# Optimization experiments

Hardware: AMD Instinct MI355X
Metric: run time of the kernel (lower is better)

Reference implementation:

```python
import jax, jax.numpy as jnp
import numpy as np

B, DIM, IMG, HEADS, DH = 8, 512, 32, 8, 64
INNER = HEADS * DH  # == DIM, required by final reshape(b, n, c)
N = IMG * IMG
BN_EPS = 1e-5


def setup_inputs() -> dict:
    key = jax.random.key(0)
    ks = jax.random.split(key, 11)
    s = lambda k, sh: jax.random.normal(k, sh, jnp.float32) * 0.05
    return {
        "x": jax.random.normal(ks[0], (B, N, DIM), jnp.float32),
        # stacked q/k/v params, index 0=q, 1=k, 2=v
        "dw_w": s(ks[1], (3, DIM, 1, 3, 3)),   # depthwise conv kernels (OIHW, groups=DIM)
        "dw_b": s(ks[2], (3, DIM)),
        "bn_g": jnp.ones((3, DIM), jnp.float32) + s(ks[3], (3, DIM)),
        "bn_b": s(ks[4], (3, DIM)),
        "bn_m": s(ks[5], (3, DIM)),
        "bn_v": jnp.abs(jax.random.normal(ks[6], (3, DIM), jnp.float32)) + 1.0,
        "pw_w": s(ks[7], (3, INNER, DIM)),     # pointwise 1x1 conv weights
        "pw_b": s(ks[8], (3, INNER)),
        "out_w": s(ks[9], (DIM, INNER)),       # nn.Linear weight [out, in]
        "out_b": s(ks[10], (DIM,)),
    }


def _proj(x_img, dw_w, dw_b, bn_g, bn_b, bn_m, bn_v, pw_w, pw_b):
    # depthwise 3x3 conv, stride 1, pad 1
    y = jax.lax.conv_general_dilated(
        x_img, dw_w, (1, 1), [(1, 1), (1, 1)],
        dimension_numbers=("NCHW", "OIHW", "NCHW"), feature_group_count=DIM)
    y = y + dw_b[None, :, None, None]
    # eval-mode BatchNorm2d
    scale = bn_g / jnp.sqrt(bn_v + BN_EPS)
    y = (y - bn_m[None, :, None, None]) * scale[None, :, None, None] + bn_b[None, :, None, None]
    # pointwise 1x1 conv
    y = jnp.einsum("bchw,oc->bohw", y, pw_w) + pw_b[None, :, None, None]
    return y


def reference(x, dw_w, dw_b, bn_g, bn_b, bn_m, bn_v, pw_w, pw_b, out_w, out_b):
    b = x.shape[0]
    # b (l w) c -> b c l w
    xi = x.transpose(0, 2, 1).reshape(b, DIM, IMG, IMG)
    # q, k, v: b (h d) l w -> b h (l w) d
    qkv = [
        _proj(xi, dw_w[i], dw_b[i], bn_g[i], bn_b[i], bn_m[i], bn_v[i], pw_w[i], pw_b[i])
        .reshape(b, HEADS, DH, N).transpose(0, 1, 3, 2)
        for i in range(3)
    ]
    q, k, v = qkv
    att = jax.nn.softmax(jnp.einsum("bhnd,bhmd->bhnm", q, k) * (DH ** -0.5), axis=-1)
    out = jnp.einsum("bhnm,bhmd->bhnd", att, v)  # [b,h,n,d]
    out = out.transpose(0, 2, 1, 3).reshape(b, N, INNER)
    return out @ out_w.T + out_b  # to_out Linear (dropout=0)
```

## Files before the change

kernel.cpp:

```cpp
#include <hip/hip_runtime.h>
#include <hip/hip_bf16.h>

#define BB    8
#define DIMC  512
#define IMGS  32
#define NPIX  1024
#define NHEAD 8
#define DHEAD 64

typedef __attribute__((ext_vector_type(8))) short short8;
typedef __attribute__((ext_vector_type(4))) float float4v;

__device__ __forceinline__ float b2f(unsigned short u) {
  union { unsigned int i; float f; } c;
  c.i = ((unsigned int)u) << 16;
  return c.f;
}
__device__ __forceinline__ unsigned short f2b(float f) {
  union { float f; unsigned int u; } c;
  c.f = f;
  unsigned int r = c.u + 0x7fffu + ((c.u >> 16) & 1u);
  return (unsigned short)(r >> 16);
}

__device__ __forceinline__ void storeC(float* p, float v) { *p = v; }
__device__ __forceinline__ void storeC(unsigned short* p, float v) { *p = f2b(v); }

__device__ __forceinline__ void async16(const void* g, void* l) {
  __builtin_amdgcn_global_load_lds(
      (const __attribute__((address_space(1))) void*)g,
      (__attribute__((address_space(3))) void*)l, 16, 0, 0);
}

#define WAITCNT_VM0   0x0F70
#define WAITCNT_LGKM0 0xC07F

__global__ __launch_bounds__(256) void wcvt_kernel(
    const float* __restrict__ pw_w, const float* __restrict__ out_w,
    const float* __restrict__ pw_b, const float* __restrict__ dw_w,
    const float* __restrict__ dw_b, const float* __restrict__ bn_g,
    const float* __restrict__ bn_b, const float* __restrict__ bn_m,
    const float* __restrict__ bn_v, unsigned short* __restrict__ wbf,
    float* __restrict__ bb, float* __restrict__ wT,
    float* __restrict__ shiftv) {
  const int i4 = (blockIdx.x * 256 + threadIdx.x) * 4;
  float4 v = (i4 < 3 * DIMC * DIMC)
                 ? *reinterpret_cast<const float4*>(pw_w + i4)
                 : *reinterpret_cast<const float4*>(out_w + (i4 - 3 * DIMC * DIMC));
  const float sc = (i4 < DIMC * DIMC) ? 0.125f : 1.0f;
  ushort4 o;
  o.x = f2b(v.x * sc); o.y = f2b(v.y * sc); o.z = f2b(v.z * sc); o.w = f2b(v.w * sc);
  *reinterpret_cast<ushort4*>(wbf + i4) = o;
  const int idx = blockIdx.x * 256 + threadIdx.x;
  if (idx < 6 * 256) {
    if (idx < 3 * DIMC / 2) {
      #pragma unroll
      for (int hh = 0; hh < 2; ++hh) {
        const int id2 = idx * 2 + hh;
        const int i = id2 >> 9, c = id2 & 511;
        const float scale = bn_g[id2] * rsqrtf(bn_v[id2] + 1e-5f);
        shiftv[id2] = (dw_b[id2] - bn_m[id2]) * scale + bn_b[id2];
        #pragma unroll
        for (int t = 0; t < 9; ++t)
          wT[(i * 9 + t) * DIMC + c] = dw_w[(size_t)id2 * 9 + t] * scale;
      }
    }
    #pragma unroll
    for (int k = 0; k < 1; ++k) {
      if (idx < 3 * DIMC)
        bb[idx] = pw_b[idx] * (idx < DIMC ? 0.125f : 1.0f);
    }
  }
}

__global__ __launch_bounds__(256) void dwbn_kernel(
    const float* __restrict__ x, const float* __restrict__ wT,
    const float* __restrict__ shiftv, unsigned short* __restrict__ z) {
  const int wp = blockIdx.x, lg = blockIdx.y, b = blockIdx.z;
  const int t = threadIdx.x;
  const int c = (t & 127) * 4;
  const int w = wp * 2 + (t >> 7);
  const int l0 = lg * 4;
  const float* xb = x + (size_t)b * NPIX * DIMC + c;

  const float4 zero4 = make_float4(0.f, 0.f, 0.f, 0.f);
  float4 win[6][3];
  #pragma unroll
  for (int rr = 0; rr < 6; ++rr) {
    const int l = l0 - 1 + rr;
    #pragma unroll
    for (int dw = 0; dw < 3; ++dw) {
      const int ww = w - 1 + dw;
      const bool ok = ((unsigned)l < IMGS) && ((unsigned)ww < IMGS);
      win[rr][dw] = ok ? *reinterpret_cast<const float4*>(
                             xb + (size_t)(l * IMGS + ww) * DIMC)
                       : zero4;
    }
  }

  #pragma unroll
  for (int i = 0; i < 3; ++i) {
    float4 wv[9];
    #pragma unroll
    for (int tp = 0; tp < 9; ++tp)
      wv[tp] = *reinterpret_cast<const float4*>(wT + (i * 9 + tp) * DIMC + c);
    const float4 sh = *reinterpret_cast<const float4*>(shiftv + i * DIMC + c);
    #pragma unroll
    for (int r = 0; r < 4; ++r) {
      float a0 = sh.x, a1 = sh.y, a2 = sh.z, a3 = sh.w;
      #pragma unroll
      for (int kh = 0; kh < 3; ++kh)
        #pragma unroll
        for (int kw = 0; kw < 3; ++kw) {
          const float4 wq = wv[kh * 3 + kw];
          const float4 xq = win[r + kh][kw];
          a0 = fmaf(wq.x, xq.x, a0);
          a1 = fmaf(wq.y, xq.y, a1);
          a2 = fmaf(wq.z, xq.z, a2);
          a3 = fmaf(wq.w, xq.w, a3);
        }
      ushort4 st;
      st.x = f2b(a0); st.y = f2b(a1); st.z = f2b(a2); st.w = f2b(a3);
      *reinterpret_cast<ushort4*>(
          z + (((size_t)(i * BB + b)) * NPIX + (l0 + r) * IMGS + w) * DIMC + c) = st;
    }
  }
}

template <typename CT>
__global__ __launch_bounds__(256) void gemm_mfma(
    const unsigned short* __restrict__ Abase,
    const unsigned short* __restrict__ Wbase,
    const float* __restrict__ biasBase, CT* __restrict__ Cbase) {
  __shared__ short As[8 * 64 * 8];
  __shared__ short Bs[8 * 64 * 8];
  const int bz = blockIdx.z;
  const int wi = bz >> 3;
  const short* A = (const short*)Abase + (size_t)bz * NPIX * DIMC;
  const short* W = (const short*)Wbase + (size_t)wi * DIMC * DIMC;
  const float* bias = biasBase + wi * DIMC;
  CT* C = Cbase + (size_t)bz * NPIX * DIMC;

  const int t = threadIdx.x;
  const int wv = t >> 6, lane = t & 63;
  const int lo = lane & 15, hi = lane >> 4;
  const int wm = wv >> 1, wn = wv & 1;
  const int m0 = blockIdx.y * 128, n0 = blockIdx.x * 128;

  float4v acc[4][4];
  #pragma unroll
  for (int i = 0; i < 4; ++i)
    #pragma unroll
    for (int j = 0; j < 4; ++j) acc[i][j] = {0.f, 0.f, 0.f, 0.f};

  for (int k0 = 0; k0 < DIMC; k0 += 32) {
    #pragma unroll
    for (int p = 0; p < 2; ++p) {
      const int sub = wv + p * 4;
      async16(A + (size_t)(m0 + sub * 16 + lo) * DIMC + k0 + hi * 8,
              As + (sub * 64 + lane) * 8);
      async16(W + (size_t)(n0 + sub * 16 + lo) * DIMC + k0 + hi * 8,
              Bs + (sub * 64 + lane) * 8);
    }
    __syncthreads();
    short8 af[4], bf[4];
    #pragma unroll
    for (int mt = 0; mt < 4; ++mt)
      af[mt] = *reinterpret_cast<const short8*>(As + ((wm * 4 + mt) * 64 + lane) * 8);
    #pragma unroll
    for (int nt = 0; nt < 4; ++nt)
      bf[nt] = *reinterpret_cast<const short8*>(Bs + ((wn * 4 + nt) * 64 + lane) * 8);
    #pragma unroll
    for (int mt = 0; mt < 4; ++mt)
      #pragma unroll
      for (int nt = 0; nt < 4; ++nt)
        acc[mt][nt] = __builtin_amdgcn_mfma_f32_16x16x32_bf16(af[mt], bf[nt],
                                                              acc[mt][nt], 0, 0, 0);
    __syncthreads();
  }

  float bv[4];
  #pragma unroll
  for (int nt = 0; nt < 4; ++nt) bv[nt] = bias[n0 + wn * 64 + nt * 16 + lo];
  #pragma unroll
  for (int mt = 0; mt < 4; ++mt) {
    #pragma unroll
    for (int r = 0; r < 4; ++r) {
      const int row = m0 + wm * 64 + mt * 16 + hi * 4 + r;
      CT* cp = C + (size_t)row * DIMC + n0 + wn * 64 + lo;
      #pragma unroll
      for (int nt = 0; nt < 4; ++nt) storeC(cp + nt * 16, acc[mt][nt][r] + bv[nt]);
    }
  }
}

__global__ __launch_bounds__(256) void vt_kernel(
    const unsigned short* __restrict__ v, unsigned short* __restrict__ vt) {
  __shared__ unsigned short tile[64][68];
  const int n0 = blockIdx.x * 64, h = blockIdx.y, b = blockIdx.z;
  const int t = threadIdx.x;
  const unsigned short* vb = v + (size_t)b * NPIX * DIMC + h * DHEAD;
  #pragma unroll
  for (int u = 0; u < 4; ++u) {
    const int lin = t + u * 256;
    const int row = lin >> 4, c4 = (lin & 15) * 4;
    *reinterpret_cast<ushort4*>(&tile[row][c4]) =
        *reinterpret_cast<const ushort4*>(vb + (size_t)(n0 + row) * DIMC + c4);
  }
  __syncthreads();
  unsigned short* vtb = vt + ((size_t)(b * NHEAD + h)) * DHEAD * NPIX;
  #pragma unroll
  for (int u = 0; u < 4; ++u) {
    const int lin = t + u * 256;
    const int d = lin >> 4, n4 = (lin & 15) * 4;
    ushort4 o;
    o.x = tile[n4 + 0][d];
    o.y = tile[n4 + 1][d];
    o.z = tile[n4 + 2][d];
    o.w = tile[n4 + 3][d];
    *reinterpret_cast<ushort4*>(vtb + (size_t)d * NPIX + n0 + n4) = o;
  }
}

__global__ __launch_bounds__(256, 2) void attn_mfma(
    const unsigned short* __restrict__ qkv, const unsigned short* __restrict__ vt,
    unsigned short* __restrict__ attn_o) {
  __shared__ char sm[53248];
  const int qt = blockIdx.x, h = blockIdx.y, b = blockIdx.z;
  const int t = threadIdx.x;
  const int wv = t >> 6, lane = t & 63;
  const int lo = lane & 15, hi = lane >> 4;

  char* wbase = sm + wv * 13312;
  short* Ks = (short*)(wbase);
  short* VTs = (short*)(wbase + 4096);
  short* Ps = (short*)(wbase + 8192);

  const short* qb = (const short*)qkv + ((size_t)(0 * BB + b) * NPIX) * DIMC + h * DHEAD;
  const short* kb = (const short*)qkv + ((size_t)(1 * BB + b) * NPIX) * DIMC + h * DHEAD;
  const short* vtb = (const short*)vt + ((size_t)(b * NHEAD + h)) * DHEAD * NPIX;

  short8 qf[4][2];
  #pragma unroll
  for (int mt = 0; mt < 4; ++mt)
    #pragma unroll
    for (int cc = 0; cc < 2; ++cc)
      qf[mt][cc] = *reinterpret_cast<const short8*>(
          qb + (size_t)(qt * 64 + mt * 16 + lo) * DIMC + cc * 32 + hi * 8);

  float4v oacc[4][4];
  float4v lsum[4];
  #pragma unroll
  for (int mt = 0; mt < 4; ++mt) {
    lsum[mt] = {0.f, 0.f, 0.f, 0.f};
    #pragma unroll
    for (int dt = 0; dt < 4; ++dt) oacc[mt][dt] = {0.f, 0.f, 0.f, 0.f};
  }

  const int n0 = wv * 256;
  for (int kt = 0; kt < 8; ++kt) {
    const int kbase = n0 + kt * 32;
    __builtin_amdgcn_s_waitcnt(WAITCNT_LGKM0);
    __builtin_amdgcn_sched_barrier(0);
    #pragma unroll
    for (int s = 0; s < 4; ++s) {
      const int nt = s >> 1, cc = s & 1;
      async16(kb + (size_t)(kbase + nt * 16 + lo) * DIMC + cc * 32 + hi * 8,
              Ks + (s * 64 + lane) * 8);
    }
    #pragma unroll
    for (int dt = 0; dt < 4; ++dt)
      async16(vtb + (size_t)(dt * 16 + lo) * NPIX + kbase + hi * 8,
              VTs + (dt * 64 + lane) * 8);
    __builtin_amdgcn_sched_barrier(0);
    __builtin_amdgcn_s_waitcnt(WAITCNT_VM0);
    __builtin_amdgcn_sched_barrier(0);

    short8 kf[2][2];
    #pragma unroll
    for (int nt = 0; nt < 2; ++nt)
      #pragma unroll
      for (int cc = 0; cc < 2; ++cc)
        kf[nt][cc] = *reinterpret_cast<const short8*>(Ks + ((nt * 2 + cc) * 64 + lane) * 8);
    float4v sacc[4][2];
    #pragma unroll
    for (int mt = 0; mt < 4; ++mt)
      #pragma unroll
      for (int nt = 0; nt < 2; ++nt) {
        sacc[mt][nt] = {0.f, 0.f, 0.f, 0.f};
        sacc[mt][nt] = __builtin_amdgcn_mfma_f32_16x16x32_bf16(qf[mt][0], kf[nt][0],
                                                               sacc[mt][nt], 0, 0, 0);
        sacc[mt][nt] = __builtin_amdgcn_mfma_f32_16x16x32_bf16(qf[mt][1], kf[nt][1],
                                                               sacc[mt][nt], 0, 0, 0);
      }

    #pragma unroll
    for (int mt = 0; mt < 4; ++mt)
      #pragma unroll
      for (int nt = 0; nt < 2; ++nt)
        #pragma unroll
        for (int r = 0; r < 4; ++r) {
          const float p = __expf(sacc[mt][nt][r]);
          Ps[(mt * 16 + hi * 4 + r) * 40 + nt * 16 + lo] = (short)f2b(p);
          lsum[mt][r] += p;
        }

    short8 vf[4];
    #pragma unroll
    for (int dt = 0; dt < 4; ++dt)
      vf[dt] = *reinterpret_cast<const short8*>(VTs + (dt * 64 + lane) * 8);
    #pragma unroll
    for (int mt = 0; mt < 4; ++mt) {
      const short8 pf = *reinterpret_cast<const short8*>(Ps + (mt * 16 + lo) * 40 + hi * 8);
      #pragma unroll
      for (int dt = 0; dt < 4; ++dt)
        oacc[mt][dt] = __builtin_amdgcn_mfma_f32_16x16x32_bf16(pf, vf[dt],
                                                               oacc[mt][dt], 0, 0, 0);
    }
  }

  #pragma unroll
  for (int mt = 0; mt < 4; ++mt)
    #pragma unroll
    for (int r = 0; r < 4; ++r) {
      float v = lsum[mt][r];
      v += __shfl_xor(v, 1);
      v += __shfl_xor(v, 2);
      v += __shfl_xor(v, 4);
      v += __shfl_xor(v, 8);
      lsum[mt][r] = v;
    }

  float* Obuf = (float*)sm;
  float* lbuf = (float*)(sm + 16384);
  float* linv = (float*)(sm + 17408);
  __syncthreads();
  if (lo == 0) {
    #pragma unroll
    for (int mt = 0; mt < 4; ++mt)
      #pragma unroll
      for (int r = 0; r < 4; ++r) lbuf[wv * 64 + mt * 16 + hi * 4 + r] = lsum[mt][r];
  }
  __syncthreads();
  if (t < 64) linv[t] = 1.0f / (lbuf[t] + lbuf[64 + t] + lbuf[128 + t] + lbuf[192 + t]);

  unsigned short* aob = attn_o + ((size_t)b * NPIX + qt * 64) * DIMC + h * DHEAD;
  #pragma unroll
  for (int mt = 0; mt < 4; ++mt) {
    __syncthreads();
    #pragma unroll
    for (int dt = 0; dt < 4; ++dt)
      #pragma unroll
      for (int r = 0; r < 4; ++r)
        Obuf[wv * 1024 + (dt * 4 + r) * 64 + lane] = oacc[mt][dt][r];
    __syncthreads();
    #pragma unroll
    for (int k2 = 0; k2 < 4; ++k2) {
      const int e = t + k2 * 256;
      const float sum2 = Obuf[e] + Obuf[1024 + e] + Obuf[2048 + e] + Obuf[3072 + e];
      const int dt = e >> 8, r = (e >> 6) & 3, le = e & 63;
      const int row = mt * 16 + (le >> 4) * 4 + r, d = dt * 16 + (le & 15);
      aob[(size_t)row * DIMC + d] = f2b(sum2 * linv[row]);
    }
  }
}

extern "C" void kernel_launch(void* const* d_in, const int* in_sizes, int n_in,
                              void* d_out, int out_size, void* d_ws, size_t ws_size,
                              hipStream_t stream) {
  const float* x    = (const float*)d_in[0];
  const float* dw_w = (const float*)d_in[1];
  const float* dw_b = (const float*)d_in[2];
  const float* bn_g = (const float*)d_in[3];
  const float* bn_b = (const float*)d_in[4];
  const float* bn_m = (const float*)d_in[5];
  const float* bn_v = (const float*)d_in[6];
  const float* pw_w = (const float*)d_in[7];
  const float* pw_b = (const float*)d_in[8];
  const float* out_w = (const float*)d_in[9];
  const float* out_b = (const float*)d_in[10];
  float* out = (float*)d_out;

  unsigned short* z   = (unsigned short*)d_ws;
  unsigned short* qkv = z + (size_t)3 * BB * NPIX * DIMC;
  unsigned short* wbf = qkv + (size_t)3 * BB * NPIX * DIMC;
  float* bb = (float*)(wbf + (size_t)4 * DIMC * DIMC);
  float* wT = bb + 3 * DIMC;
  float* shiftv = wT + 3 * 9 * DIMC;
  unsigned short* vtb = z;
  unsigned short* attn_o = z + (size_t)BB * NHEAD * DHEAD * NPIX;

  wcvt_kernel<<<dim3(1024), 256, 0, stream>>>(pw_w, out_w, pw_b, dw_w, dw_b,
                                              bn_g, bn_b, bn_m, bn_v, wbf, bb,
                                              wT, shiftv);
  dwbn_kernel<<<dim3(16, 8, BB), 256, 0, stream>>>(x, wT, shiftv, z);
  gemm_mfma<unsigned short><<<dim3(4, 8, 24), 256, 0, stream>>>(z, wbf, bb, qkv);
  vt_kernel<<<dim3(16, NHEAD, BB), 256, 0, stream>>>(
      qkv + (size_t)2 * BB * NPIX * DIMC, vtb);
  attn_mfma<<<dim3(16, NHEAD, BB), 256, 0, stream>>>(qkv, vtb, attn_o);
  gemm_mfma<float><<<dim3(4, 8, 8), 256, 0, stream>>>(
      attn_o, wbf + (size_t)3 * DIMC * DIMC, out_b, out);
}
```

Before: 204.9 us.

## Register double-buffer K/V loads in attention and use exp2 with folded log2e scale

Replaces the per-iteration async global-to-LDS K/V staging with direct global loads into registers. The loads are double-buffered so the next key tile is fetched while the current one is computed, and the loop is fully unrolled. The loop-scoped waitcnt barriers are removed and the LDS allocation shrinks to only the P buffer, which could raise occupancy. The query scale now folds log2(e) in so softmax can use exp2f, and P uses a cheaper round-half-up bf16 conversion. In exchange, register pressure rises and bf16 rounding changes slightly.

New measurement: 234.4 us. 1.14x slower.

```diff
diff --git a/kernel.cpp b/kernel.cpp
--- a/kernel.cpp
+++ b/kernel.cpp
@@ -8,6 +8,8 @@
 #define NHEAD 8
 #define DHEAD 64
 
+#define QSC 0.18033688011112043f
+
 typedef __attribute__((ext_vector_type(8))) short short8;
 typedef __attribute__((ext_vector_type(4))) float float4v;
 
@@ -22,6 +24,11 @@
   unsigned int r = c.u + 0x7fffu + ((c.u >> 16) & 1u);
   return (unsigned short)(r >> 16);
 }
+__device__ __forceinline__ unsigned short f2b_fast(float f) {
+  union { float f; unsigned int u; } c;
+  c.f = f;
+  return (unsigned short)((c.u + 0x8000u) >> 16);
+}
 
 __device__ __forceinline__ void storeC(float* p, float v) { *p = v; }
 __device__ __forceinline__ void storeC(unsigned short* p, float v) { *p = f2b(v); }
@@ -31,9 +38,6 @@
       (const __attribute__((address_space(1))) void*)g,
       (__attribute__((address_space(3))) void*)l, 16, 0, 0);
 }
-
-#define WAITCNT_VM0   0x0F70
-#define WAITCNT_LGKM0 0xC07F
 
 __global__ __launch_bounds__(256) void wcvt_kernel(
     const float* __restrict__ pw_w, const float* __restrict__ out_w,
@@ -47,7 +51,7 @@
   float4 v = (i4 < 3 * DIMC * DIMC)
                  ? *reinterpret_cast<const float4*>(pw_w + i4)
                  : *reinterpret_cast<const float4*>(out_w + (i4 - 3 * DIMC * DIMC));
-  const float sc = (i4 < DIMC * DIMC) ? 0.125f : 1.0f;
+  const float sc = (i4 < DIMC * DIMC) ? QSC : 1.0f;
   ushort4 o;
   o.x = f2b(v.x * sc); o.y = f2b(v.y * sc); o.z = f2b(v.z * sc); o.w = f2b(v.w * sc);
   *reinterpret_cast<ushort4*>(wbf + i4) = o;
@@ -68,7 +72,7 @@
     #pragma unroll
     for (int k = 0; k < 1; ++k) {
       if (idx < 3 * DIMC)
-        bb[idx] = pw_b[idx] * (idx < DIMC ? 0.125f : 1.0f);
+        bb[idx] = pw_b[idx] * (idx < DIMC ? QSC : 1.0f);
     }
   }
 }
@@ -222,19 +226,65 @@
   }
 }
 
+__device__ __forceinline__ void load_kf(const short* kb, int kbase, int lo,
+                                        int hi, short8 (&kf)[2][2]) {
+  #pragma unroll
+  for (int nt = 0; nt < 2; ++nt)
+    #pragma unroll
+    for (int cc = 0; cc < 2; ++cc)
+      kf[nt][cc] = *reinterpret_cast<const short8*>(
+          kb + (size_t)(kbase + nt * 16 + lo) * DIMC + cc * 32 + hi * 8);
+}
+__device__ __forceinline__ void load_vf(const short* vtb, int kbase, int lo,
+                                        int hi, short8 (&vf)[4]) {
+  #pragma unroll
+  for (int dt = 0; dt < 4; ++dt)
+    vf[dt] = *reinterpret_cast<const short8*>(
+        vtb + (size_t)(dt * 16 + lo) * NPIX + kbase + hi * 8);
+}
+
+#define ATTN_STEP(KF, VF, KN, VN, KT)                                          \
+  {                                                                            \
+    if ((KT) < 7) {                                                            \
+      load_kf(kb, n0 + ((KT) + 1) * 32, lo, hi, KN);                           \
+      load_vf(vtb, n0 + ((KT) + 1) * 32, lo, hi, VN);                          \
+    }                                                                          \
+    float4v sacc[4][2];                                                        \
+    _Pragma("unroll") for (int mt = 0; mt < 4; ++mt)                           \
+      _Pragma("unroll") for (int nt = 0; nt < 2; ++nt) {                       \
+        sacc[mt][nt] = {0.f, 0.f, 0.f, 0.f};                                   \
+        sacc[mt][nt] = __builtin_amdgcn_mfma_f32_16x16x32_bf16(                \
+            qf[mt][0], KF[nt][0], sacc[mt][nt], 0, 0, 0);                      \
+        sacc[mt][nt] = __builtin_amdgcn_mfma_f32_16x16x32_bf16(                \
+            qf[mt][1], KF[nt][1], sacc[mt][nt], 0, 0, 0);                      \
+      }                                                                        \
+    _Pragma("unroll") for (int mt = 0; mt < 4; ++mt)                           \
+      _Pragma("unroll") for (int nt = 0; nt < 2; ++nt)                         \
+        _Pragma("unroll") for (int r = 0; r < 4; ++r) {                        \
+          const float p = exp2f(sacc[mt][nt][r]);                              \
+          Ps[(mt * 16 + hi * 4 + r) * 40 + nt * 16 + lo] =                     \
+              (short)f2b_fast(p);                                             \
+          lsum[mt][r] += p;                                                    \
+        }                                                                      \
+    _Pragma("unroll") for (int mt = 0; mt < 4; ++mt) {                         \
+      const short8 pf = *reinterpret_cast<const short8*>(                      \
+          Ps + (mt * 16 + lo) * 40 + hi * 8);                                  \
+      _Pragma("unroll") for (int dt = 0; dt < 4; ++dt)                         \
+        oacc[mt][dt] = __builtin_amdgcn_mfma_f32_16x16x32_bf16(                \
+            pf, VF[dt], oacc[mt][dt], 0, 0, 0);                                \
+    }                                                                          \
+  }
+
 __global__ __launch_bounds__(256, 2) void attn_mfma(
     const unsigned short* __restrict__ qkv, const unsigned short* __restrict__ vt,
     unsigned short* __restrict__ attn_o) {
-  __shared__ char sm[53248];
+  __shared__ __align__(16) char sm[20480];
   const int qt = blockIdx.x, h = blockIdx.y, b = blockIdx.z;
   const int t = threadIdx.x;
   const int wv = t >> 6, lane = t & 63;
   const int lo = lane & 15, hi = lane >> 4;
 
-  char* wbase = sm + wv * 13312;
-  short* Ks = (short*)(wbase);
-  short* VTs = (short*)(wbase + 4096);
-  short* Ps = (short*)(wbase + 8192);
+  short* Ps = (short*)(sm + wv * 5120);
 
   const short* qb = (const short*)qkv + ((size_t)(0 * BB + b) * NPIX) * DIMC + h * DHEAD;
   const short* kb = (const short*)qkv + ((size_t)(1 * BB + b) * NPIX) * DIMC + h * DHEAD;
@@ -258,65 +308,14 @@
   }
 
   const int n0 = wv * 256;
-  for (int kt = 0; kt < 8; ++kt) {
-    const int kbase = n0 + kt * 32;
-    __builtin_amdgcn_s_waitcnt(WAITCNT_LGKM0);
-    __builtin_amdgcn_sched_barrier(0);
-    #pragma unroll
-    for (int s = 0; s < 4; ++s) {
-      const int nt = s >> 1, cc = s & 1;
-      async16(kb + (size_t)(kbase + nt * 16 + lo) * DIMC + cc * 32 + hi * 8,
-              Ks + (s * 64 + lane) * 8);
-    }
-    #pragma unroll
-    for (int dt = 0; dt < 4; ++dt)
-      async16(vtb + (size_t)(dt * 16 + lo) * NPIX + kbase + hi * 8,
-              VTs + (dt * 64 + lane) * 8);
-    __builtin_amdgcn_sched_barrier(0);
-    __builtin_amdgcn_s_waitcnt(WAITCNT_VM0);
-    __builtin_amdgcn_sched_barrier(0);
-
-    short8 kf[2][2];
-    #pragma unroll
-    for (int nt = 0; nt < 2; ++nt)
-      #pragma unroll
-      for (int cc = 0; cc < 2; ++cc)
-        kf[nt][cc] = *reinterpret_cast<const short8*>(Ks + ((nt * 2 + cc) * 64 + lane) * 8);
-    float4v sacc[4][2];
-    #pragma unroll
-    for (int mt = 0; mt < 4; ++mt)
-      #pragma unroll
-      for (int nt = 0; nt < 2; ++nt) {
-        sacc[mt][nt] = {0.f, 0.f, 0.f, 0.f};
-        sacc[mt][nt] = __builtin_amdgcn_mfma_f32_16x16x32_bf16(qf[mt][0], kf[nt][0],
-                                                               sacc[mt][nt], 0, 0, 0);
-        sacc[mt][nt] = __builtin_amdgcn_mfma_f32_16x16x32_bf16(qf[mt][1], kf[nt][1],
-                                                               sacc[mt][nt], 0, 0, 0);
-      }
-
-    #pragma unroll
-    for (int mt = 0; mt < 4; ++mt)
-      #pragma unroll
-      for (int nt = 0; nt < 2; ++nt)
-        #pragma unroll
-        for (int r = 0; r < 4; ++r) {
-          const float p = __expf(sacc[mt][nt][r]);
-          Ps[(mt * 16 + hi * 4 + r) * 40 + nt * 16 + lo] = (short)f2b(p);
-          lsum[mt][r] += p;
-        }
-
-    short8 vf[4];
-    #pragma unroll
-    for (int dt = 0; dt < 4; ++dt)
-      vf[dt] = *reinterpret_cast<const short8*>(VTs + (dt * 64 + lane) * 8);
-    #pragma unroll
-    for (int mt = 0; mt < 4; ++mt) {
-      const short8 pf = *reinterpret_cast<const short8*>(Ps + (mt * 16 + lo) * 40 + hi * 8);
-      #pragma unroll
-      for (int dt = 0; dt < 4; ++dt)
-        oacc[mt][dt] = __builtin_amdgcn_mfma_f32_16x16x32_bf16(pf, vf[dt],
-                                                               oacc[mt][dt], 0, 0, 0);
-    }
+
+  short8 kbufA[2][2], kbufB[2][2], vbufA[4], vbufB[4];
+  load_kf(kb, n0, lo, hi, kbufA);
+  load_vf(vtb, n0, lo, hi, vbufA);
+  #pragma unroll
+  for (int kt2 = 0; kt2 < 4; ++kt2) {
+    ATTN_STEP(kbufA, vbufA, kbufB, vbufB, kt2 * 2);
+    ATTN_STEP(kbufB, vbufB, kbufA, vbufA, kt2 * 2 + 1);
   }
 
   #pragma unroll
```

## Double-buffer K tiles, load V directly to registers, use exp2 softmax

Applied to the files above, without the earlier changes.

The attention loop now prefetches the next K tile into a second LDS buffer while computing the current one. V fragments are loaded straight from global memory into registers instead of going through LDS. The Q scale now folds in log2(e), so exp2f replaces __expf, and the probabilities are rounded to bf16 with a cheaper conversion. This is meant to hide global-load latency and cut ALU work in the softmax, at the cost of more registers and slightly different rounding.

After: 227.3 us. 10.9% more time.

```diff
diff --git a/kernel.cpp b/kernel.cpp
--- a/kernel.cpp
+++ b/kernel.cpp
@@ -8,6 +8,8 @@
 #define NHEAD 8
 #define DHEAD 64
 
+#define QSC 0.18033688011112043f
+
 typedef __attribute__((ext_vector_type(8))) short short8;
 typedef __attribute__((ext_vector_type(4))) float float4v;
 
@@ -22,6 +24,11 @@
   unsigned int r = c.u + 0x7fffu + ((c.u >> 16) & 1u);
   return (unsigned short)(r >> 16);
 }
+__device__ __forceinline__ unsigned short f2b_fast(float f) {
+  union { float f; unsigned int u; } c;
+  c.f = f;
+  return (unsigned short)((c.u + 0x8000u) >> 16);
+}
 
 __device__ __forceinline__ void storeC(float* p, float v) { *p = v; }
 __device__ __forceinline__ void storeC(unsigned short* p, float v) { *p = f2b(v); }
@@ -33,6 +40,8 @@
 }
 
 #define WAITCNT_VM0   0x0F70
+#define WAITCNT_VM4   0x0F74
+#define WAITCNT_VM8   0x0F78
 #define WAITCNT_LGKM0 0xC07F
 
 __global__ __launch_bounds__(256) void wcvt_kernel(
@@ -47,7 +56,7 @@
   float4 v = (i4 < 3 * DIMC * DIMC)
                  ? *reinterpret_cast<const float4*>(pw_w + i4)
                  : *reinterpret_cast<const float4*>(out_w + (i4 - 3 * DIMC * DIMC));
-  const float sc = (i4 < DIMC * DIMC) ? 0.125f : 1.0f;
+  const float sc = (i4 < DIMC * DIMC) ? QSC : 1.0f;
   ushort4 o;
   o.x = f2b(v.x * sc); o.y = f2b(v.y * sc); o.z = f2b(v.z * sc); o.w = f2b(v.w * sc);
   *reinterpret_cast<ushort4*>(wbf + i4) = o;
@@ -68,7 +77,7 @@
     #pragma unroll
     for (int k = 0; k < 1; ++k) {
       if (idx < 3 * DIMC)
-        bb[idx] = pw_b[idx] * (idx < DIMC ? 0.125f : 1.0f);
+        bb[idx] = pw_b[idx] * (idx < DIMC ? QSC : 1.0f);
     }
   }
 }
@@ -225,16 +234,16 @@
 __global__ __launch_bounds__(256, 2) void attn_mfma(
     const unsigned short* __restrict__ qkv, const unsigned short* __restrict__ vt,
     unsigned short* __restrict__ attn_o) {
-  __shared__ char sm[53248];
+  __shared__ __align__(16) char sm[53248];
   const int qt = blockIdx.x, h = blockIdx.y, b = blockIdx.z;
   const int t = threadIdx.x;
   const int wv = t >> 6, lane = t & 63;
   const int lo = lane & 15, hi = lane >> 4;
 
   char* wbase = sm + wv * 13312;
-  short* Ks = (short*)(wbase);
-  short* VTs = (short*)(wbase + 4096);
-  short* Ps = (short*)(wbase + 8192);
+  short* Ks0 = (short*)(wbase);
+  short* Ks1 = (short*)(wbase + 4096);
+  short* Ps  = (short*)(wbase + 8192);
 
   const short* qb = (const short*)qkv + ((size_t)(0 * BB + b) * NPIX) * DIMC + h * DHEAD;
   const short* kb = (const short*)qkv + ((size_t)(1 * BB + b) * NPIX) * DIMC + h * DHEAD;
@@ -258,57 +267,65 @@
   }
 
   const int n0 = wv * 256;
+
+  #pragma unroll
+  for (int s = 0; s < 4; ++s) {
+    const int nt = s >> 1, cc = s & 1;
+    async16(kb + (size_t)(n0 + nt * 16 + lo) * DIMC + cc * 32 + hi * 8,
+            Ks0 + (s * 64 + lane) * 8);
+  }
+
+  #pragma unroll
   for (int kt = 0; kt < 8; ++kt) {
+    short* Kc = (kt & 1) ? Ks1 : Ks0;
+    short* Kn = (kt & 1) ? Ks0 : Ks1;
     const int kbase = n0 + kt * 32;
-    __builtin_amdgcn_s_waitcnt(WAITCNT_LGKM0);
+
+    short8 vf[4];
+    #pragma unroll
+    for (int dt = 0; dt < 4; ++dt)
+      vf[dt] = *reinterpret_cast<const short8*>(
+          vtb + (size_t)(dt * 16 + lo) * NPIX + kbase + hi * 8);
+
+    if (kt < 7) {
+      __builtin_amdgcn_s_waitcnt(WAITCNT_LGKM0);
+      __builtin_amdgcn_sched_barrier(0);
+      #pragma unroll
+      for (int s = 0; s < 4; ++s) {
+        const int nt = s >> 1, cc = s & 1;
+        async16(kb + (size_t)(kbase + 32 + nt * 16 + lo) * DIMC + cc * 32 + hi * 8,
+                Kn + (s * 64 + lane) * 8);
+      }
+      __builtin_amdgcn_sched_barrier(0);
+      __builtin_amdgcn_s_waitcnt(WAITCNT_VM8);
+    } else {
+      __builtin_amdgcn_s_waitcnt(WAITCNT_VM4);
+    }
     __builtin_amdgcn_sched_barrier(0);
-    #pragma unroll
-    for (int s = 0; s < 4; ++s) {
-      const int nt = s >> 1, cc = s & 1;
-      async16(kb + (size_t)(kbase + nt * 16 + lo) * DIMC + cc * 32 + hi * 8,
-              Ks + (s * 64 + lane) * 8);
-    }
-    #pragma unroll
-    for (int dt = 0; dt < 4; ++dt)
-      async16(vtb + (size_t)(dt * 16 + lo) * NPIX + kbase + hi * 8,
-              VTs + (dt * 64 + lane) * 8);
-    __builtin_amdgcn_sched_barrier(0);
-    __builtin_amdgcn_s_waitcnt(WAITCNT_VM0);
-    __builtin_amdgcn_sched_barrier(0);
 
     short8 kf[2][2];
     #pragma unroll
     for (int nt = 0; nt < 2; ++nt)
       #pragma unroll
       for (int cc = 0; cc < 2; ++cc)
-        kf[nt][cc] = *reinterpret_cast<const short8*>(Ks + ((nt * 2 + cc) * 64 + lane) * 8);
-    float4v sacc[4][2];
-    #pragma unroll
-    for (int mt = 0; mt < 4; ++mt)
-      #pragma unroll
-      for (int nt = 0; nt < 2; ++nt) {
-        sacc[mt][nt] = {0.f, 0.f, 0.f, 0.f};
-        sacc[mt][nt] = __builtin_amdgcn_mfma_f32_16x16x32_bf16(qf[mt][0], kf[nt][0],
-                                                               sacc[mt][nt], 0, 0, 0);
-        sacc[mt][nt] = __builtin_amdgcn_mfma_f32_16x16x32_bf16(qf[mt][1], kf[nt][1],
-                                                               sacc[mt][nt], 0, 0, 0);
+        kf[nt][cc] = *reinterpret_cast<const short8*>(Kc + ((nt * 2 + cc) * 64 + lane) * 8);
+    #pragma unroll
+    for (int mt = 0; mt < 4; ++mt) {
+      float4v s0 = {0.f, 0.f, 0.f, 0.f}, s1 = {0.f, 0.f, 0.f, 0.f};
+      s0 = __builtin_amdgcn_mfma_f32_16x16x32_bf16(qf[mt][0], kf[0][0], s0, 0, 0, 0);
+      s0 = __builtin_amdgcn_mfma_f32_16x16x32_bf16(qf[mt][1], kf[0][1], s0, 0, 0, 0);
+      s1 = __builtin_amdgcn_mfma_f32_16x16x32_bf16(qf[mt][0], kf[1][0], s1, 0, 0, 0);
+      s1 = __builtin_amdgcn_mfma_f32_16x16x32_bf16(qf[mt][1], kf[1][1], s1, 0, 0, 0);
+      #pragma unroll
+      for (int r = 0; r < 4; ++r) {
+        const float p0 = exp2f(s0[r]);
+        const float p1 = exp2f(s1[r]);
+        Ps[(mt * 16 + hi * 4 + r) * 40 + lo] = (short)f2b_fast(p0);
+        Ps[(mt * 16 + hi * 4 + r) * 40 + 16 + lo] = (short)f2b_fast(p1);
+        lsum[mt][r] += p0 + p1;
       }
-
-    #pragma unroll
-    for (int mt = 0; mt < 4; ++mt)
-      #pragma unroll
-      for (int nt = 0; nt < 2; ++nt)
-        #pragma unroll
-        for (int r = 0; r < 4; ++r) {
-          const float p = __expf(sacc[mt][nt][r]);
-          Ps[(mt * 16 + hi * 4 + r) * 40 + nt * 16 + lo] = (short)f2b(p);
-          lsum[mt][r] += p;
-        }
-
-    short8 vf[4];
-    #pragma unroll
-    for (int dt = 0; dt < 4; ++dt)
-      vf[dt] = *reinterpret_cast<const short8*>(VTs + (dt * 64 + lane) * 8);
+    }
+
     #pragma unroll
     for (int mt = 0; mt < 4; ++mt) {
       const short8 pf = *reinterpret_cast<const short8*>(Ps + (mt * 16 + lo) * 40 + hi * 8);
```

## Use exp2 with log2e-folded Q scale, transposed score MFMA, packed bf16 P stores

Applied to the files above, without the earlier changes.

Folds log2(e) into the Q projection scale so softmax numerators can use exp2f instead of expf. Swaps the MFMA operand order so each lane holds a transposed score fragment, which lets P be written as packed bf16 pairs with v_cvt_pk_bf16_f32 and cuts the row-sum reduction to two shuffles. It also flattens the grid so blocks sharing a query tile launch together, and raises the occupancy hint to 3 blocks per CU. The softmax still has no max subtraction, so it keeps the existing overflow risk, and the higher occupancy target may pressure registers.

Measured after the change: 203.5 us. About the same (-0.7%).

```diff
diff --git a/kernel.cpp b/kernel.cpp
--- a/kernel.cpp
+++ b/kernel.cpp
@@ -8,6 +8,8 @@
 #define NHEAD 8
 #define DHEAD 64
 
+#define QSC 0.18033688011112043f
+
 typedef __attribute__((ext_vector_type(8))) short short8;
 typedef __attribute__((ext_vector_type(4))) float float4v;
 
@@ -21,6 +23,11 @@
   c.f = f;
   unsigned int r = c.u + 0x7fffu + ((c.u >> 16) & 1u);
   return (unsigned short)(r >> 16);
+}
+__device__ __forceinline__ unsigned int cvt_pk_bf16(float a, float b) {
+  unsigned int r;
+  asm("v_cvt_pk_bf16_f32 %0, %1, %2" : "=v"(r) : "v"(a), "v"(b));
+  return r;
 }
 
 __device__ __forceinline__ void storeC(float* p, float v) { *p = v; }
@@ -47,7 +54,7 @@
   float4 v = (i4 < 3 * DIMC * DIMC)
                  ? *reinterpret_cast<const float4*>(pw_w + i4)
                  : *reinterpret_cast<const float4*>(out_w + (i4 - 3 * DIMC * DIMC));
-  const float sc = (i4 < DIMC * DIMC) ? 0.125f : 1.0f;
+  const float sc = (i4 < DIMC * DIMC) ? QSC : 1.0f;
   ushort4 o;
   o.x = f2b(v.x * sc); o.y = f2b(v.y * sc); o.z = f2b(v.z * sc); o.w = f2b(v.w * sc);
   *reinterpret_cast<ushort4*>(wbf + i4) = o;
@@ -68,7 +75,7 @@
     #pragma unroll
     for (int k = 0; k < 1; ++k) {
       if (idx < 3 * DIMC)
-        bb[idx] = pw_b[idx] * (idx < DIMC ? 0.125f : 1.0f);
+        bb[idx] = pw_b[idx] * (idx < DIMC ? QSC : 1.0f);
     }
   }
 }
@@ -222,19 +229,21 @@
   }
 }
 
-__global__ __launch_bounds__(256, 2) void attn_mfma(
+__global__ __launch_bounds__(256, 3) void attn_mfma(
     const unsigned short* __restrict__ qkv, const unsigned short* __restrict__ vt,
     unsigned short* __restrict__ attn_o) {
   __shared__ char sm[53248];
-  const int qt = blockIdx.x, h = blockIdx.y, b = blockIdx.z;
+  const int hb = blockIdx.x & 63;
+  const int qt = blockIdx.x >> 6;
+  const int h = hb & 7, b = hb >> 3;
   const int t = threadIdx.x;
   const int wv = t >> 6, lane = t & 63;
   const int lo = lane & 15, hi = lane >> 4;
 
   char* wbase = sm + wv * 13312;
-  short* Ks = (short*)(wbase);
+  short* Ks  = (short*)(wbase);
   short* VTs = (short*)(wbase + 4096);
-  short* Ps = (short*)(wbase + 8192);
+  short* Ps  = (short*)(wbase + 8192);
 
   const short* qb = (const short*)qkv + ((size_t)(0 * BB + b) * NPIX) * DIMC + h * DHEAD;
   const short* kb = (const short*)qkv + ((size_t)(1 * BB + b) * NPIX) * DIMC + h * DHEAD;
@@ -249,15 +258,17 @@
           qb + (size_t)(qt * 64 + mt * 16 + lo) * DIMC + cc * 32 + hi * 8);
 
   float4v oacc[4][4];
-  float4v lsum[4];
+  float lsum[4];
   #pragma unroll
   for (int mt = 0; mt < 4; ++mt) {
-    lsum[mt] = {0.f, 0.f, 0.f, 0.f};
+    lsum[mt] = 0.f;
     #pragma unroll
     for (int dt = 0; dt < 4; ++dt) oacc[mt][dt] = {0.f, 0.f, 0.f, 0.f};
   }
 
   const int n0 = wv * 256;
+  short* PsW = Ps + lo * 40 + hi * 4;
+
   for (int kt = 0; kt < 8; ++kt) {
     const int kbase = n0 + kt * 32;
     __builtin_amdgcn_s_waitcnt(WAITCNT_LGKM0);
@@ -288,22 +299,29 @@
       #pragma unroll
       for (int nt = 0; nt < 2; ++nt) {
         sacc[mt][nt] = {0.f, 0.f, 0.f, 0.f};
-        sacc[mt][nt] = __builtin_amdgcn_mfma_f32_16x16x32_bf16(qf[mt][0], kf[nt][0],
+        sacc[mt][nt] = __builtin_amdgcn_mfma_f32_16x16x32_bf16(kf[nt][0], qf[mt][0],
                                                                sacc[mt][nt], 0, 0, 0);
-        sacc[mt][nt] = __builtin_amdgcn_mfma_f32_16x16x32_bf16(qf[mt][1], kf[nt][1],
+        sacc[mt][nt] = __builtin_amdgcn_mfma_f32_16x16x32_bf16(kf[nt][1], qf[mt][1],
                                                                sacc[mt][nt], 0, 0, 0);
       }
 
     #pragma unroll
-    for (int mt = 0; mt < 4; ++mt)
-      #pragma unroll
-      for (int nt = 0; nt < 2; ++nt)
-        #pragma unroll
-        for (int r = 0; r < 4; ++r) {
-          const float p = __expf(sacc[mt][nt][r]);
-          Ps[(mt * 16 + hi * 4 + r) * 40 + nt * 16 + lo] = (short)f2b(p);
-          lsum[mt][r] += p;
-        }
+    for (int mt = 0; mt < 4; ++mt) {
+      const float p00 = exp2f(sacc[mt][0][0]);
+      const float p01 = exp2f(sacc[mt][0][1]);
+      const float p02 = exp2f(sacc[mt][0][2]);
+      const float p03 = exp2f(sacc[mt][0][3]);
+      const float p10 = exp2f(sacc[mt][1][0]);
+      const float p11 = exp2f(sacc[mt][1][1]);
+      const float p12 = exp2f(sacc[mt][1][2]);
+      const float p13 = exp2f(sacc[mt][1][3]);
+      uint2 w0, w1;
+      w0.x = cvt_pk_bf16(p00, p01); w0.y = cvt_pk_bf16(p02, p03);
+      w1.x = cvt_pk_bf16(p10, p11); w1.y = cvt_pk_bf16(p12, p13);
+      *reinterpret_cast<uint2*>(PsW + mt * 640) = w0;
+      *reinterpret_cast<uint2*>(PsW + mt * 640 + 16) = w1;
+      lsum[mt] += ((p00 + p01) + (p02 + p03)) + ((p10 + p11) + (p12 + p13));
+    }
 
     short8 vf[4];
     #pragma unroll
@@ -319,27 +337,22 @@
     }
   }
 
-  #pragma unroll
-  for (int mt = 0; mt < 4; ++mt)
-    #pragma unroll
-    for (int r = 0; r < 4; ++r) {
-      float v = lsum[mt][r];
-      v += __shfl_xor(v, 1);
-      v += __shfl_xor(v, 2);
-      v += __shfl_xor(v, 4);
-      v += __shfl_xor(v, 8);
-      lsum[mt][r] = v;
-    }
+  float lv[4];
+  #pragma unroll
+  for (int mt = 0; mt < 4; ++mt) {
+    float v = lsum[mt];
+    v += __shfl_xor(v, 16);
+    v += __shfl_xor(v, 32);
+    lv[mt] = v;
+  }
 
   float* Obuf = (float*)sm;
   float* lbuf = (float*)(sm + 16384);
   float* linv = (float*)(sm + 17408);
   __syncthreads();
-  if (lo == 0) {
-    #pragma unroll
-    for (int mt = 0; mt < 4; ++mt)
-      #pragma unroll
-      for (int r = 0; r < 4; ++r) lbuf[wv * 64 + mt * 16 + hi * 4 + r] = lsum[mt][r];
+  if (hi == 0) {
+    #pragma unroll
+    for (int mt = 0; mt < 4; ++mt) lbuf[wv * 64 + mt * 16 + lo] = lv[mt];
   }
   __syncthreads();
   if (t < 64) linv[t] = 1.0f / (lbuf[t] + lbuf[64 + t] + lbuf[128 + t] + lbuf[192 + t]);
@@ -397,7 +410,7 @@
   gemm_mfma<unsigned short><<<dim3(4, 8, 24), 256, 0, stream>>>(z, wbf, bb, qkv);
   vt_kernel<<<dim3(16, NHEAD, BB), 256, 0, stream>>>(
       qkv + (size_t)2 * BB * NPIX * DIMC, vtb);
-  attn_mfma<<<dim3(16, NHEAD, BB), 256, 0, stream>>>(qkv, vtb, attn_o);
+  attn_mfma<<<dim3(1024), 256, 0, stream>>>(qkv, vtb, attn_o);
   gemm_mfma<float><<<dim3(4, 8, 8), 256, 0, stream>>>(
       attn_o, wbf + (size_t)3 * DIMC * DIMC, out_b, out);
 }
```
